# Kernel tuning notes

Measured on AMD Instinct MI355X. Metric: run time of the kernel, lower is better.

Reference implementation:

```python
import jax, jax.numpy as jnp
import numpy as np

B, D, ND, N2, H = 16384, 512, 4, 32, 4
C = D  # attention channels (per-detector feature dim)
EPS = 1e-5


def setup_inputs() -> dict:
    key = jax.random.key(0)
    ks = jax.random.split(key, 8)
    rn = lambda k, s, sc: jax.random.normal(k, s, jnp.float32) * sc
    return {
        'x': jax.random.normal(ks[0], (B, D), jnp.float32),
        'bn1_g': jnp.ones(D * ND, jnp.float32), 'bn1_b': jnp.zeros(D * ND, jnp.float32),
        'w1': rn(ks[1], (ND, D, D), 1e-4),  # diagonal blocks of the masked EnsembleLinear weight
        'bn2_g': jnp.ones(D * ND, jnp.float32), 'bn2_b': jnp.zeros(D * ND, jnp.float32),
        'wq': rn(ks[2], (C, D), 0.02), 'bq': jnp.zeros(C, jnp.float32),
        'wk': rn(ks[3], (C, D), 0.02), 'bk': jnp.zeros(C, jnp.float32),
        'wv': rn(ks[4], (C, D), 0.02), 'bv': jnp.zeros(C, jnp.float32),
        'wo': rn(ks[5], (C, C), 0.02), 'bo': jnp.zeros(C, jnp.float32),
        'ln1_g': jnp.ones(C, jnp.float32), 'ln1_b': jnp.zeros(C, jnp.float32),
        'wff': rn(ks[6], (C, C), 0.02), 'bff': jnp.zeros(C, jnp.float32),
        'ln2_g': jnp.ones(C, jnp.float32), 'ln2_b': jnp.zeros(C, jnp.float32),
        'w2': rn(ks[7], (ND, N2, D), 1e-4),
        'bn3_g': jnp.ones(N2 * ND, jnp.float32), 'bn3_b': jnp.zeros(N2 * ND, jnp.float32),
    }


def _batchnorm(x, g, b):
    # training-mode BatchNorm1d: biased batch stats over the batch axis
    m = x.mean(0)
    v = ((x - m) ** 2).mean(0)
    return (x - m) * jax.lax.rsqrt(v + EPS) * g + b


def _layernorm(x, g, b):
    m = x.mean(-1, keepdims=True)
    v = ((x - m) ** 2).mean(-1, keepdims=True)
    return (x - m) * jax.lax.rsqrt(v + EPS) * g + b


def reference(x, bn1_g, bn1_b, w1, bn2_g, bn2_b, wq, bq, wk, bk, wv, bv, wo, bo,
              ln1_g, ln1_b, wff, bff, ln2_g, ln2_b, w2, bn3_g, bn3_b):
    n = x.shape[0]
    # concat x num_detectors times along features: [n, ND*D]
    xc = jnp.tile(x, (1, ND))
    h = _batchnorm(xc, bn1_g, bn1_b)
    # EnsembleLinear 1: block-diagonal masked matmul == one small GEMM per detector
    h = jnp.einsum('ndi,doi->ndo', h.reshape(n, ND, D), w1).reshape(n, ND * D)
    h = jax.nn.sigmoid(_batchnorm(h, bn2_g, bn2_b))
    # 4-token self-attention over detectors: t is [n, ND, D]
    t = h.reshape(n, ND, D)
    hd = C // H
    q = (t @ wq.T + bq).reshape(n, ND, H, hd).transpose(0, 2, 1, 3)  # [n,H,S,hd]
    k = (t @ wk.T + bk).reshape(n, ND, H, hd).transpose(0, 2, 1, 3)
    v = (t @ wv.T + bv).reshape(n, ND, H, hd).transpose(0, 2, 1, 3)
    scale = jnp.sqrt(jnp.float32(C / H))
    scores = jnp.einsum('nhqd,nhkd->nhqk', q, k) / scale
    attn = jax.nn.softmax(scores, axis=-1)
    o = jnp.einsum('nhqk,nhkd->nhqd', attn, v).transpose(0, 2, 1, 3).reshape(n, ND, C)
    o = o @ wo.T + bo
    a1 = _layernorm(o + t, ln1_g, ln1_b)
    a2 = _layernorm(a1 @ wff.T + bff + a1, ln2_g, ln2_b)
    # EnsembleLinear 2: per-detector D -> N2
    h2 = jnp.einsum('ndi,doi->ndo', a2, w2).reshape(n, ND * N2)
    out = jax.nn.sigmoid(_batchnorm(h2, bn3_g, bn3_b))
    return out
```

## Files before the change

### kernel.cpp

```cpp
#include <hip/hip_runtime.h>
#include <hip/hip_bf16.h>

#define EPS 1e-5f

typedef __attribute__((ext_vector_type(8))) short bf16x8;
typedef __attribute__((ext_vector_type(4))) float f32x4;
typedef __attribute__((ext_vector_type(4))) float float4v;

__device__ __forceinline__ float b2f(short u) {
    union { unsigned int i; float f; } x;
    x.i = ((unsigned int)(unsigned short)u) << 16;
    return x.f;
}
__device__ __forceinline__ short f2b(float f) {
    unsigned int x = __builtin_bit_cast(unsigned int, f);
    unsigned int r = (x + 0x7FFFu + ((x >> 16) & 1u)) >> 16;
    return (short)r;
}

__device__ __forceinline__ void load_lds16(const void* g, void* l) {
    __builtin_amdgcn_global_load_lds(
        (const __attribute__((address_space(1))) unsigned int*)g,
        (__attribute__((address_space(3))) unsigned int*)l, 16, 0, 0);
}


__global__ __launch_bounds__(256) void k_cast_bf16(const float* __restrict__ src,
                                                   short* __restrict__ dst, int n8) {
    int i = blockIdx.x * 256 + threadIdx.x;
    if (i >= n8) return;
    const float4v* s = (const float4v*)src;
    float4v a = s[(long)i * 2], b = s[(long)i * 2 + 1];
    bf16x8 o;
    o[0] = f2b(a[0]); o[1] = f2b(a[1]); o[2] = f2b(a[2]); o[3] = f2b(a[3]);
    o[4] = f2b(b[0]); o[5] = f2b(b[1]); o[6] = f2b(b[2]); o[7] = f2b(b[3]);
    *(bf16x8*)(dst + (long)i * 8) = o;
}

__global__ void k_concat3(const float* __restrict__ a, const float* __restrict__ b,
                          const float* __restrict__ c, float* __restrict__ dst) {
    int i = blockIdx.x * 256 + threadIdx.x;
    if (i < 512) dst[i] = a[i];
    else if (i < 1024) dst[i] = b[i - 512];
    else if (i < 1536) dst[i] = c[i - 1024];
}

__global__ __launch_bounds__(256) void k_stats_x(const float* __restrict__ x,
                                                 float* __restrict__ psum, float* __restrict__ psq) {
    int b = blockIdx.x, tid = threadIdx.x;
    const float* xp = x + (long)b * 64 * 512;
    float s0 = 0, q0 = 0, s1 = 0, q1 = 0;
    for (int r = 0; r < 64; ++r) {
        float v0 = xp[r * 512 + tid];
        float v1 = xp[r * 512 + tid + 256];
        s0 += v0; q0 += v0 * v0; s1 += v1; q1 += v1 * v1;
    }
    psum[b * 512 + tid] = s0; psum[b * 512 + tid + 256] = s1;
    psq[b * 512 + tid] = q0;  psq[b * 512 + tid + 256] = q1;
}


__global__ __launch_bounds__(256) void k_finalize_meanrs(const float* __restrict__ psum,
                                                         const float* __restrict__ psq,
                                                         int nparts, int ncols, float invB,
                                                         float* __restrict__ mean, float* __restrict__ rs) {
    int l = threadIdx.x & 63, grp = threadIdx.x >> 6;
    int c = blockIdx.x * 64 + l;
    float s = 0, q = 0;
    for (int p = grp; p < nparts; p += 4) {
        s += psum[(long)p * ncols + c];
        q += psq[(long)p * ncols + c];
    }
    __shared__ float rs_[4][64], rq_[4][64];
    rs_[grp][l] = s; rq_[grp][l] = q;
    __syncthreads();
    if (grp == 0) {
        s = rs_[0][l] + rs_[1][l] + rs_[2][l] + rs_[3][l];
        q = rq_[0][l] + rq_[1][l] + rq_[2][l] + rq_[3][l];
        float m = s * invB;
        float v = q * invB - m * m;
        mean[c] = m;
        rs[c] = rsqrtf(v + EPS);
    }
}

__global__ __launch_bounds__(256) void k_finalize_ss(const float* __restrict__ psum,
                                                     const float* __restrict__ psq,
                                                     int nparts, int ncols, float invB,
                                                     const float* __restrict__ g, const float* __restrict__ bb,
                                                     float* __restrict__ scale, float* __restrict__ shift) {
    int l = threadIdx.x & 63, grp = threadIdx.x >> 6;
    int c = blockIdx.x * 64 + l;
    float s = 0, q = 0;
    for (int p = grp; p < nparts; p += 4) {
        s += psum[(long)p * ncols + c];
        q += psq[(long)p * ncols + c];
    }
    __shared__ float rs_[4][64], rq_[4][64];
    rs_[grp][l] = s; rq_[grp][l] = q;
    __syncthreads();
    if (grp == 0) {
        s = rs_[0][l] + rs_[1][l] + rs_[2][l] + rs_[3][l];
        q = rq_[0][l] + rq_[1][l] + rq_[2][l] + rq_[3][l];
        float m = s * invB, v = q * invB - m * m;
        float sc = g[c] * rsqrtf(v + EPS);
        scale[c] = sc;
        shift[c] = bb[c] - m * sc;
    }
}

__global__ __launch_bounds__(256) void k_fold_w1(const float* __restrict__ w1, const float* __restrict__ g1,
                                                 const float* __restrict__ b1, const float* __restrict__ mean,
                                                 const float* __restrict__ rs,
                                                 short* __restrict__ W1b, float* __restrict__ beff) {
    int bx = blockIdx.x;
    int d = bx >> 9, tid = threadIdx.x;
    const float* wrow = w1 + (long)bx * 512;
    float part = 0.f;
    for (int i = tid; i < 512; i += 256) {
        float wv = wrow[i];
        float sc = rs[i] * g1[d * 512 + i];
        W1b[(long)bx * 512 + i] = f2b(wv * sc);
        part += (b1[d * 512 + i] - mean[i] * sc) * wv;
    }
    __shared__ float red[256];
    red[tid] = part;
    __syncthreads();
    for (int st = 128; st > 0; st >>= 1) {
        if (tid < st) red[tid] += red[tid + st];
        __syncthreads();
    }
    if (tid == 0) beff[bx] = red[0];
}

__global__ __launch_bounds__(256) void k_stats_h(const short* __restrict__ h,
                                                 float* __restrict__ psum, float* __restrict__ psq) {
    int b = blockIdx.x, tid = threadIdx.x;
    const short* hp = h + (long)b * 64 * 2048;
    float s[8] = {0, 0, 0, 0, 0, 0, 0, 0}, q[8] = {0, 0, 0, 0, 0, 0, 0, 0};
    int c0 = tid * 8;
    for (int r = 0; r < 64; ++r) {
        bf16x8 v = *(const bf16x8*)(hp + r * 2048 + c0);
#pragma unroll
        for (int j = 0; j < 8; ++j) { float f = b2f(v[j]); s[j] += f; q[j] += f * f; }
    }
#pragma unroll
    for (int j = 0; j < 8; ++j) {
        psum[(long)b * 2048 + c0 + j] = s[j];
        psq[(long)b * 2048 + c0 + j] = q[j];
    }
}

__global__ __launch_bounds__(256) void k_bnsig(const short* h, short* t,
                                               const float* __restrict__ scale,
                                               const float* __restrict__ shift) {
    long i8 = ((long)blockIdx.x * 256 + threadIdx.x) * 8;
    int c0 = (int)(i8 & 2047);
    bf16x8 v = *(const bf16x8*)(h + i8);
    bf16x8 o;
#pragma unroll
    for (int j = 0; j < 8; ++j) {
        float x = b2f(v[j]) * scale[c0 + j] + shift[c0 + j];
        o[j] = f2b(1.f / (1.f + __expf(-x)));
    }
    *(bf16x8*)(t + i8) = o;
}

__global__ __launch_bounds__(256) void k_ln(const short* in, short* out,
                                            const float* __restrict__ g, const float* __restrict__ bb) {
    int w = threadIdx.x >> 6, lane = threadIdx.x & 63;
    long row = (long)blockIdx.x * 4 + w;
    const short* rp = in + row * 512;
    bf16x8 v = *(const bf16x8*)(rp + lane * 8);
    float f[8];
    float s = 0.f;
#pragma unroll
    for (int j = 0; j < 8; ++j) { f[j] = b2f(v[j]); s += f[j]; }
#pragma unroll
    for (int m = 1; m < 64; m <<= 1) s += __shfl_xor(s, m, 64);
    float mean = s * (1.f / 512.f);
    float q = 0.f;
#pragma unroll
    for (int j = 0; j < 8; ++j) { float d = f[j] - mean; q += d * d; }
#pragma unroll
    for (int m = 1; m < 64; m <<= 1) q += __shfl_xor(q, m, 64);
    float rs = rsqrtf(q * (1.f / 512.f) + EPS);
    bf16x8 o;
#pragma unroll
    for (int j = 0; j < 8; ++j) {
        int c = lane * 8 + j;
        o[j] = f2b((f[j] - mean) * rs * g[c] + bb[c]);
    }
    *(bf16x8*)(out + row * 512 + lane * 8) = o;
}

__global__ __launch_bounds__(256) void k_stats_o(const float* __restrict__ pre,
                                                 float* __restrict__ psum, float* __restrict__ psq) {
    int b = blockIdx.x, tid = threadIdx.x;
    int c = tid & 127, rh = tid >> 7;
    const float* pp = pre + (long)b * 128 * 128;
    float s = 0, q = 0;
    for (int r = rh; r < 128; r += 2) {
        float v = pp[r * 128 + c];
        s += v; q += v * v;
    }
    psum[(b * 2 + rh) * 128 + c] = s;
    psq[(b * 2 + rh) * 128 + c] = q;
}

__global__ __launch_bounds__(256) void k_bn3sig(const float* __restrict__ pre, float* __restrict__ out,
                                                const float* __restrict__ scale, const float* __restrict__ shift) {
    long i4 = ((long)blockIdx.x * 256 + threadIdx.x) * 4;
    float4v v = *(const float4v*)(pre + i4);
    int c0 = (int)(i4 & 127);
    float4v o;
#pragma unroll
    for (int j = 0; j < 4; ++j) {
        float x = v[j] * scale[c0 + j] + shift[c0 + j];
        o[j] = 1.f / (1.f + __expf(-x));
    }
    *(float4v*)(out + i4) = o;
}


template <int BM, int BN, int WGM, int WGN, bool ADD_RES, bool OUT_BF16>
__global__ __launch_bounds__(WGM* WGN * 64) void k_gemm_bt(
    const short* __restrict__ A, int a_zoff, int lda,
    const short* __restrict__ W, int w_zoff,
    const float* __restrict__ bias, int bias_zoff,
    short* __restrict__ Cb, float* __restrict__ Cf, int c_zoff, int ldc,
    const short* __restrict__ R, int ldr, int K) {
    constexpr int BK = 32;
    constexpr int WM = BM / WGM, WN = BN / WGN;
    constexpr int AM = WM / 16, AN = WN / 16;
    constexpr int NT = WGM * WGN * 64;
    constexpr int CH = (BM + BN) * (BK / 8);

    __shared__ alignas(16) short Smem[(BM + BN) * BK];

    int tid = threadIdx.x;
    int wave = tid >> 6, lane = tid & 63;
    int wm = (wave % WGM) * WM, wn = (wave / WGM) * WN;
    long m0 = (long)blockIdx.x * BM;
    int n0 = blockIdx.y * BN;
    int z = blockIdx.z;
    const short* Az = A + (long)z * a_zoff;
    const short* Wz = W + (long)z * w_zoff;

    f32x4 acc[AM][AN];
#pragma unroll
    for (int i = 0; i < AM; ++i)
#pragma unroll
        for (int j = 0; j < AN; ++j)
#pragma unroll
            for (int q = 0; q < 4; ++q) acc[i][j][q] = 0.f;

    int fr = lane & 15, ko = (lane >> 4) * 8;

    for (int k0 = 0; k0 < K; k0 += BK) {
#pragma unroll
        for (int c = tid; c < CH; c += NT) {
            int row = c >> 2, koff = (c & 3) * 8;
            const short* g = (row < BM) ? (Az + (m0 + row) * lda + k0 + koff)
                                        : (Wz + (long)(n0 + row - BM) * K + k0 + koff);
            load_lds16(g, (char*)Smem + (size_t)c * 16);
        }
        __syncthreads();
        bf16x8 af[AM], bfr[AN];
#pragma unroll
        for (int i = 0; i < AM; ++i) af[i] = *(const bf16x8*)(&Smem[(wm + i * 16 + fr) * BK + ko]);
#pragma unroll
        for (int j = 0; j < AN; ++j) bfr[j] = *(const bf16x8*)(&Smem[(BM + wn + j * 16 + fr) * BK + ko]);
#pragma unroll
        for (int i = 0; i < AM; ++i)
#pragma unroll
            for (int j = 0; j < AN; ++j)
                acc[i][j] = __builtin_amdgcn_mfma_f32_16x16x32_bf16(af[i], bfr[j], acc[i][j], 0, 0, 0);
        __syncthreads();
    }

    int cr = (lane >> 4) * 4, cc = lane & 15;
#pragma unroll
    for (int i = 0; i < AM; ++i) {
#pragma unroll
        for (int j = 0; j < AN; ++j) {
            int col = n0 + wn + j * 16 + cc;
            float bv = bias ? bias[(long)z * bias_zoff + col] : 0.f;
#pragma unroll
            for (int q = 0; q < 4; ++q) {
                long row = m0 + wm + i * 16 + cr + q;
                float v = acc[i][j][q] + bv;
                if constexpr (ADD_RES) v += b2f(R[row * (long)ldr + col]);
                long idx = row * (long)ldc + (long)z * c_zoff + col;
                if constexpr (OUT_BF16) Cb[idx] = f2b(v);
                else Cf[idx] = v;
            }
        }
    }
}

__global__ __launch_bounds__(256) void k_attn(const short* __restrict__ qkv, short* __restrict__ ao) {
    __shared__ alignas(16) short lds[4][4][1544];
    __shared__ float attn_s[4][4][4][4];
    int w = threadIdx.x >> 6, lane = threadIdx.x & 63;
    long n = (long)blockIdx.x * 4 + w;
    const short* src = qkv + n * 4 * 1536;
#pragma unroll
    for (int c = 0; c < 12; ++c) {
        int e = c * 512 + lane * 8;
        *(bf16x8*)(&lds[w][e / 1536][e % 1536]) = *(const bf16x8*)(src + e);
    }
    __syncthreads();
    int h = lane >> 4, a = (lane >> 2) & 3, b = lane & 3;
    const short* qp = &lds[w][a][h * 128];
    const short* kp = &lds[w][b][512 + h * 128];
    float s = 0.f;
#pragma unroll
    for (int j = 0; j < 128; j += 8) {
        bf16x8 qv = *(const bf16x8*)(qp + j);
        bf16x8 kv = *(const bf16x8*)(kp + j);
#pragma unroll
        for (int x = 0; x < 8; ++x) s += b2f(qv[x]) * b2f(kv[x]);
    }
    s *= 0.08838834764831845f;
    float mx = fmaxf(s, __shfl_xor(s, 1, 64));
    mx = fmaxf(mx, __shfl_xor(mx, 2, 64));
    float e = __expf(s - mx);
    float den = e + __shfl_xor(e, 1, 64);
    den += __shfl_xor(den, 2, 64);
    attn_s[w][h][a][b] = e / den;
    __syncthreads();
    int ta = lane >> 4, cg = lane & 15;
#pragma unroll
    for (int hh = 0; hh < 4; ++hh) {
        int c0 = hh * 128 + cg * 8;
        float at0 = attn_s[w][hh][ta][0], at1 = attn_s[w][hh][ta][1];
        float at2 = attn_s[w][hh][ta][2], at3 = attn_s[w][hh][ta][3];
        bf16x8 v0 = *(const bf16x8*)(&lds[w][0][1024 + c0]);
        bf16x8 v1 = *(const bf16x8*)(&lds[w][1][1024 + c0]);
        bf16x8 v2 = *(const bf16x8*)(&lds[w][2][1024 + c0]);
        bf16x8 v3 = *(const bf16x8*)(&lds[w][3][1024 + c0]);
        bf16x8 ov;
#pragma unroll
        for (int j = 0; j < 8; ++j) {
            float val = at0 * b2f(v0[j]) + at1 * b2f(v1[j]) + at2 * b2f(v2[j]) + at3 * b2f(v3[j]);
            ov[j] = f2b(val);
        }
        *(bf16x8*)(ao + (n * 4 + ta) * 512 + c0) = ov;
    }
}


extern "C" void kernel_launch(void* const* d_in, const int* in_sizes, int n_in,
                              void* d_out, int out_size, void* d_ws, size_t ws_size,
                              hipStream_t stream) {
    const float* x = (const float*)d_in[0];
    const float* bn1_g = (const float*)d_in[1];
    const float* bn1_b = (const float*)d_in[2];
    const float* w1 = (const float*)d_in[3];
    const float* bn2_g = (const float*)d_in[4];
    const float* bn2_b = (const float*)d_in[5];
    const float* wq = (const float*)d_in[6];
    const float* bq = (const float*)d_in[7];
    const float* wk = (const float*)d_in[8];
    const float* bk = (const float*)d_in[9];
    const float* wv = (const float*)d_in[10];
    const float* bv = (const float*)d_in[11];
    const float* wo = (const float*)d_in[12];
    const float* bo = (const float*)d_in[13];
    const float* ln1_g = (const float*)d_in[14];
    const float* ln1_b = (const float*)d_in[15];
    const float* wff = (const float*)d_in[16];
    const float* bff = (const float*)d_in[17];
    const float* ln2_g = (const float*)d_in[18];
    const float* ln2_b = (const float*)d_in[19];
    const float* w2 = (const float*)d_in[20];
    const float* bn3_g = (const float*)d_in[21];
    const float* bn3_b = (const float*)d_in[22];
    float* out = (float*)d_out;

    char* ws = (char*)d_ws;
    size_t off = 0;
    auto alloc = [&](size_t bytes) {
        void* p = ws + off;
        off = (off + bytes + 255) & ~(size_t)255;
        return p;
    };

    short* W1b = (short*)alloc(4l * 512 * 512 * 2);
    float* beff = (float*)alloc(4l * 512 * 4);
    short* Wqkvb = (short*)alloc(1536l * 512 * 2);
    float* bqkv = (float*)alloc(1536l * 4);
    short* wo_b = (short*)alloc(512l * 512 * 2);
    short* wff_b = (short*)alloc(512l * 512 * 2);
    short* w2_b = (short*)alloc(4l * 32 * 512 * 2);
    float* mean1 = (float*)alloc(512 * 4);
    float* rs1 = (float*)alloc(512 * 4);
    float* scale2 = (float*)alloc(2048 * 4);
    float* shift2 = (float*)alloc(2048 * 4);
    float* scale3 = (float*)alloc(128 * 4);
    float* shift3 = (float*)alloc(128 * 4);
    float* psum1 = (float*)alloc(256l * 512 * 4);
    float* psq1 = (float*)alloc(256l * 512 * 4);
    float* psum2 = (float*)alloc(256l * 2048 * 4);
    float* psq2 = (float*)alloc(256l * 2048 * 4);
    float* psum3 = (float*)alloc(256l * 128 * 4);
    float* psq3 = (float*)alloc(256l * 128 * 4);
    short* slotA = (short*)alloc(16384l * 2048 * 2);
    float* out_pre = (float*)alloc(16384l * 128 * 4);

    long NC = 1024;
    for (long cand = 16384; cand >= 1024; cand >>= 1) {
        if (off + (size_t)cand * 24576 + (1u << 20) <= ws_size) { NC = cand; break; }
    }
    char* arena = (char*)alloc((size_t)NC * 24576);
    short* xb = (short*)arena;
    short* qkv_c = (short*)arena;
    short* attn_c = (short*)(arena + (size_t)NC * 12288);
    short* a1_c = attn_c + (size_t)NC * 2048;
    short* a2_c = a1_c + (size_t)NC * 2048;

    dim3 B256(256);

    hipLaunchKernelGGL(k_cast_bf16, dim3(4096), B256, 0, stream, x, xb, 8388608 / 8);
    hipLaunchKernelGGL(k_cast_bf16, dim3(128), B256, 0, stream, wq, Wqkvb, 262144 / 8);
    hipLaunchKernelGGL(k_cast_bf16, dim3(128), B256, 0, stream, wk, Wqkvb + 262144, 262144 / 8);
    hipLaunchKernelGGL(k_cast_bf16, dim3(128), B256, 0, stream, wv, Wqkvb + 524288, 262144 / 8);
    hipLaunchKernelGGL(k_cast_bf16, dim3(128), B256, 0, stream, wo, wo_b, 262144 / 8);
    hipLaunchKernelGGL(k_cast_bf16, dim3(128), B256, 0, stream, wff, wff_b, 262144 / 8);
    hipLaunchKernelGGL(k_cast_bf16, dim3(32), B256, 0, stream, w2, w2_b, 65536 / 8);
    hipLaunchKernelGGL(k_concat3, dim3(6), B256, 0, stream, bq, bk, bv, bqkv);

    hipLaunchKernelGGL(k_stats_x, dim3(256), B256, 0, stream, x, psum1, psq1);
    hipLaunchKernelGGL(k_finalize_meanrs, dim3(8), B256, 0, stream, psum1, psq1, 256, 512,
                       1.f / 16384.f, mean1, rs1);
    hipLaunchKernelGGL(k_fold_w1, dim3(2048), B256, 0, stream, w1, bn1_g, bn1_b, mean1, rs1, W1b, beff);

    hipLaunchKernelGGL((k_gemm_bt<128, 128, 2, 2, false, true>), dim3(128, 4, 4), B256, 0, stream,
                       xb, 0, 512, W1b, 512 * 512, beff, 512,
                       slotA, (float*)nullptr, 512, 2048, (const short*)nullptr, 0, 512);

    hipLaunchKernelGGL(k_stats_h, dim3(256), B256, 0, stream, slotA, psum2, psq2);
    hipLaunchKernelGGL(k_finalize_ss, dim3(32), B256, 0, stream, psum2, psq2, 256, 2048,
                       1.f / 16384.f, bn2_g, bn2_b, scale2, shift2);
    hipLaunchKernelGGL(k_bnsig, dim3(16384), B256, 0, stream, slotA, slotA, scale2, shift2);

    long nch = 16384 / NC;
    for (long c = 0; c < nch; ++c) {
        long r0 = c * NC;
        const short* t_c = slotA + r0 * 2048;
        int gx = (int)(NC * 4 / 128);

        hipLaunchKernelGGL((k_gemm_bt<128, 128, 2, 2, false, true>), dim3(gx, 12, 1), B256, 0, stream,
                           t_c, 0, 512, Wqkvb, 0, bqkv, 0,
                           qkv_c, (float*)nullptr, 0, 1536, (const short*)nullptr, 0, 512);

        hipLaunchKernelGGL(k_attn, dim3((int)(NC / 4)), B256, 0, stream, qkv_c, attn_c);

        hipLaunchKernelGGL((k_gemm_bt<128, 128, 2, 2, true, true>), dim3(gx, 4, 1), B256, 0, stream,
                           attn_c, 0, 512, wo_b, 0, bo, 0,
                           a1_c, (float*)nullptr, 0, 512, t_c, 512, 512);

        hipLaunchKernelGGL(k_ln, dim3((int)NC), B256, 0, stream, a1_c, a1_c, ln1_g, ln1_b);

        hipLaunchKernelGGL((k_gemm_bt<128, 128, 2, 2, true, true>), dim3(gx, 4, 1), B256, 0, stream,
                           a1_c, 0, 512, wff_b, 0, bff, 0,
                           a2_c, (float*)nullptr, 0, 512, a1_c, 512, 512);

        hipLaunchKernelGGL(k_ln, dim3((int)NC), B256, 0, stream, a2_c, a2_c, ln2_g, ln2_b);

        hipLaunchKernelGGL((k_gemm_bt<128, 32, 4, 1, false, false>), dim3((int)(NC / 128), 1, 4), B256, 0, stream,
                           a2_c, 512, 2048, w2_b, 32 * 512, (const float*)nullptr, 0,
                           (short*)nullptr, out_pre + r0 * 128, 32, 128, (const short*)nullptr, 0, 512);
    }

    hipLaunchKernelGGL(k_stats_o, dim3(128), B256, 0, stream, out_pre, psum3, psq3);
    hipLaunchKernelGGL(k_finalize_ss, dim3(2), B256, 0, stream, psum3, psq3, 256, 128,
                       1.f / 16384.f, bn3_g, bn3_b, scale3, shift3);
    hipLaunchKernelGGL(k_bn3sig, dim3(2048), B256, 0, stream, out_pre, out, scale3, shift3);
}
```

Before: 657.6 us.

## Fuse BN stats into GEMM epilogues and LayerNorm into full-row GEMMs

Folds the bf16 cast of x into its column-statistics kernel, and computes BN2 partial sums and squares inside a dedicated first-layer GEMM epilogue, which removes the separate pass over h. Adds a full-row (128x512) GEMM kernel with 512 threads that adds bias and residual and applies LayerNorm in its epilogue. This replaces the wo and wff GEMMs plus their standalone LN kernels and removes intermediate round trips through memory. In exchange, the LN kernel keeps a large accumulator set per thread, which may lower occupancy, and it computes the variance as E[x^2]-mean^2 in one pass.

```diff
diff --git a/kernel.cpp b/kernel.cpp
--- a/kernel.cpp
+++ b/kernel.cpp
@@ -45,14 +45,18 @@
     else if (i < 1536) dst[i] = c[i - 1024];
 }
 
-__global__ __launch_bounds__(256) void k_stats_x(const float* __restrict__ x,
-                                                 float* __restrict__ psum, float* __restrict__ psq) {
+__global__ __launch_bounds__(256) void k_statcast_x(const float* __restrict__ x,
+                                                    short* __restrict__ xb,
+                                                    float* __restrict__ psum, float* __restrict__ psq) {
     int b = blockIdx.x, tid = threadIdx.x;
     const float* xp = x + (long)b * 64 * 512;
+    short* xo = xb + (long)b * 64 * 512;
     float s0 = 0, q0 = 0, s1 = 0, q1 = 0;
     for (int r = 0; r < 64; ++r) {
         float v0 = xp[r * 512 + tid];
         float v1 = xp[r * 512 + tid + 256];
+        xo[r * 512 + tid] = f2b(v0);
+        xo[r * 512 + tid + 256] = f2b(v1);
         s0 += v0; q0 += v0 * v0; s1 += v1; q1 += v1 * v1;
     }
     psum[b * 512 + tid] = s0; psum[b * 512 + tid + 256] = s1;
@@ -133,24 +137,6 @@
     if (tid == 0) beff[bx] = red[0];
 }
 
-__global__ __launch_bounds__(256) void k_stats_h(const short* __restrict__ h,
-                                                 float* __restrict__ psum, float* __restrict__ psq) {
-    int b = blockIdx.x, tid = threadIdx.x;
-    const short* hp = h + (long)b * 64 * 2048;
-    float s[8] = {0, 0, 0, 0, 0, 0, 0, 0}, q[8] = {0, 0, 0, 0, 0, 0, 0, 0};
-    int c0 = tid * 8;
-    for (int r = 0; r < 64; ++r) {
-        bf16x8 v = *(const bf16x8*)(hp + r * 2048 + c0);
-#pragma unroll
-        for (int j = 0; j < 8; ++j) { float f = b2f(v[j]); s[j] += f; q[j] += f * f; }
-    }
-#pragma unroll
-    for (int j = 0; j < 8; ++j) {
-        psum[(long)b * 2048 + c0 + j] = s[j];
-        psq[(long)b * 2048 + c0 + j] = q[j];
-    }
-}
-
 __global__ __launch_bounds__(256) void k_bnsig(const short* h, short* t,
                                                const float* __restrict__ scale,
                                                const float* __restrict__ shift) {
@@ -164,34 +150,6 @@
         o[j] = f2b(1.f / (1.f + __expf(-x)));
     }
     *(bf16x8*)(t + i8) = o;
-}
-
-__global__ __launch_bounds__(256) void k_ln(const short* in, short* out,
-                                            const float* __restrict__ g, const float* __restrict__ bb) {
-    int w = threadIdx.x >> 6, lane = threadIdx.x & 63;
-    long row = (long)blockIdx.x * 4 + w;
-    const short* rp = in + row * 512;
-    bf16x8 v = *(const bf16x8*)(rp + lane * 8);
-    float f[8];
-    float s = 0.f;
-#pragma unroll
-    for (int j = 0; j < 8; ++j) { f[j] = b2f(v[j]); s += f[j]; }
-#pragma unroll
-    for (int m = 1; m < 64; m <<= 1) s += __shfl_xor(s, m, 64);
-    float mean = s * (1.f / 512.f);
-    float q = 0.f;
-#pragma unroll
-    for (int j = 0; j < 8; ++j) { float d = f[j] - mean; q += d * d; }
-#pragma unroll
-    for (int m = 1; m < 64; m <<= 1) q += __shfl_xor(q, m, 64);
-    float rs = rsqrtf(q * (1.f / 512.f) + EPS);
-    bf16x8 o;
-#pragma unroll
-    for (int j = 0; j < 8; ++j) {
-        int c = lane * 8 + j;
-        o[j] = f2b((f[j] - mean) * rs * g[c] + bb[c]);
-    }
-    *(bf16x8*)(out + row * 512 + lane * 8) = o;
 }
 
 __global__ __launch_bounds__(256) void k_stats_o(const float* __restrict__ pre,
@@ -223,13 +181,12 @@
 }
 
 
-template <int BM, int BN, int WGM, int WGN, bool ADD_RES, bool OUT_BF16>
+template <int BM, int BN, int WGM, int WGN, bool OUT_BF16>
 __global__ __launch_bounds__(WGM* WGN * 64) void k_gemm_bt(
     const short* __restrict__ A, int a_zoff, int lda,
     const short* __restrict__ W, int w_zoff,
     const float* __restrict__ bias, int bias_zoff,
-    short* __restrict__ Cb, float* __restrict__ Cf, int c_zoff, int ldc,
-    const short* __restrict__ R, int ldr, int K) {
+    short* __restrict__ Cb, float* __restrict__ Cf, int c_zoff, int ldc, int K) {
     constexpr int BK = 32;
     constexpr int WM = BM / WGM, WN = BN / WGN;
     constexpr int AM = WM / 16, AN = WN / 16;
@@ -290,10 +247,183 @@
             for (int q = 0; q < 4; ++q) {
                 long row = m0 + wm + i * 16 + cr + q;
                 float v = acc[i][j][q] + bv;
-                if constexpr (ADD_RES) v += b2f(R[row * (long)ldr + col]);
                 long idx = row * (long)ldc + (long)z * c_zoff + col;
                 if constexpr (OUT_BF16) Cb[idx] = f2b(v);
                 else Cf[idx] = v;
+            }
+        }
+    }
+}
+
+
+__global__ __launch_bounds__(256) void k_gemm_e1(
+    const short* __restrict__ A, const short* __restrict__ W1, const float* __restrict__ beff,
+    short* __restrict__ h, float* __restrict__ psum, float* __restrict__ psq) {
+    constexpr int BK = 32;
+    __shared__ alignas(16) short Smem[256 * BK];
+    __shared__ float cS[2][128], cQ[2][128];
+
+    int tid = threadIdx.x;
+    int wave = tid >> 6, lane = tid & 63;
+    int wm = (wave & 1) * 64, wn = (wave >> 1) * 64;
+    long m0 = (long)blockIdx.x * 128;
+    int n0 = blockIdx.y * 128;
+    int z = blockIdx.z;
+    const short* Wz = W1 + (long)z * 512 * 512;
+
+    f32x4 acc[4][4];
+#pragma unroll
+    for (int i = 0; i < 4; ++i)
+#pragma unroll
+        for (int j = 0; j < 4; ++j)
+#pragma unroll
+            for (int q = 0; q < 4; ++q) acc[i][j][q] = 0.f;
+
+    int fr = lane & 15, ko = (lane >> 4) * 8;
+
+    for (int k0 = 0; k0 < 512; k0 += BK) {
+#pragma unroll
+        for (int c = tid; c < 1024; c += 256) {
+            int row = c >> 2, koff = (c & 3) * 8;
+            const short* g = (row < 128) ? (A + (m0 + row) * 512 + k0 + koff)
+                                         : (Wz + (long)(n0 + row - 128) * 512 + k0 + koff);
+            load_lds16(g, (char*)Smem + (size_t)c * 16);
+        }
+        __syncthreads();
+        bf16x8 af[4], bfr[4];
+#pragma unroll
+        for (int i = 0; i < 4; ++i) af[i] = *(const bf16x8*)(&Smem[(wm + i * 16 + fr) * BK + ko]);
+#pragma unroll
+        for (int j = 0; j < 4; ++j) bfr[j] = *(const bf16x8*)(&Smem[(128 + wn + j * 16 + fr) * BK + ko]);
+#pragma unroll
+        for (int i = 0; i < 4; ++i)
+#pragma unroll
+            for (int j = 0; j < 4; ++j)
+                acc[i][j] = __builtin_amdgcn_mfma_f32_16x16x32_bf16(af[i], bfr[j], acc[i][j], 0, 0, 0);
+        __syncthreads();
+    }
+
+    int cr = (lane >> 4) * 4, cc = lane & 15;
+#pragma unroll
+    for (int j = 0; j < 4; ++j) {
+        int cl = wn + j * 16 + cc;
+        float bv = beff[z * 512 + n0 + cl];
+        float s = 0.f, qq = 0.f;
+#pragma unroll
+        for (int i = 0; i < 4; ++i)
+#pragma unroll
+            for (int q = 0; q < 4; ++q) {
+                float v = acc[i][j][q] + bv;
+                acc[i][j][q] = v;
+                s += v; qq += v * v;
+                long row = m0 + wm + i * 16 + cr + q;
+                h[row * 2048 + z * 512 + n0 + cl] = f2b(v);
+            }
+        s += __shfl_xor(s, 16, 64); s += __shfl_xor(s, 32, 64);
+        qq += __shfl_xor(qq, 16, 64); qq += __shfl_xor(qq, 32, 64);
+        if (lane < 16) { cS[wave & 1][cl] = s; cQ[wave & 1][cl] = qq; }
+    }
+    __syncthreads();
+    if (tid < 128) {
+        float S = cS[0][tid] + cS[1][tid];
+        float Q = cQ[0][tid] + cQ[1][tid];
+        psum[(long)blockIdx.x * 2048 + z * 512 + n0 + tid] = S;
+        psq[(long)blockIdx.x * 2048 + z * 512 + n0 + tid] = Q;
+    }
+}
+
+
+__global__ __launch_bounds__(512) void k_gemm_ln(
+    const short* __restrict__ A, const short* __restrict__ W,
+    const float* __restrict__ bias, const short* __restrict__ R,
+    const float* __restrict__ g, const float* __restrict__ bb,
+    short* __restrict__ out) {
+    constexpr int BK = 32;
+    __shared__ alignas(16) short Smem[(128 + 512) * BK];
+    __shared__ float lnS[128][4], lnQ[128][4];
+
+    int tid = threadIdx.x;
+    int wave = tid >> 6, lane = tid & 63;
+    int wm = (wave & 1) * 64;
+    int wc = wave >> 1;
+    int wn = wc * 128;
+    long m0 = (long)blockIdx.x * 128;
+
+    f32x4 acc[4][8];
+#pragma unroll
+    for (int i = 0; i < 4; ++i)
+#pragma unroll
+        for (int j = 0; j < 8; ++j)
+#pragma unroll
+            for (int q = 0; q < 4; ++q) acc[i][j][q] = 0.f;
+
+    int fr = lane & 15, ko = (lane >> 4) * 8;
+
+    for (int k0 = 0; k0 < 512; k0 += BK) {
+#pragma unroll
+        for (int c = tid; c < 2560; c += 512) {
+            int row = c >> 2, koff = (c & 3) * 8;
+            const short* gp = (row < 128) ? (A + (m0 + row) * 512 + k0 + koff)
+                                          : (W + (long)(row - 128) * 512 + k0 + koff);
+            load_lds16(gp, (char*)Smem + (size_t)c * 16);
+        }
+        __syncthreads();
+        bf16x8 af[4], bfr[8];
+#pragma unroll
+        for (int i = 0; i < 4; ++i) af[i] = *(const bf16x8*)(&Smem[(wm + i * 16 + fr) * BK + ko]);
+#pragma unroll
+        for (int j = 0; j < 8; ++j) bfr[j] = *(const bf16x8*)(&Smem[(128 + wn + j * 16 + fr) * BK + ko]);
+#pragma unroll
+        for (int i = 0; i < 4; ++i)
+#pragma unroll
+            for (int j = 0; j < 8; ++j)
+                acc[i][j] = __builtin_amdgcn_mfma_f32_16x16x32_bf16(af[i], bfr[j], acc[i][j], 0, 0, 0);
+        __syncthreads();
+    }
+
+    int cr = (lane >> 4) * 4, cc = lane & 15;
+    float bj[8];
+#pragma unroll
+    for (int j = 0; j < 8; ++j) bj[j] = bias[wn + j * 16 + cc];
+
+#pragma unroll
+    for (int i = 0; i < 4; ++i) {
+#pragma unroll
+        for (int q = 0; q < 4; ++q) {
+            long row = m0 + wm + i * 16 + cr + q;
+            float s = 0.f, qq = 0.f;
+#pragma unroll
+            for (int j = 0; j < 8; ++j) {
+                float v = acc[i][j][q] + bj[j] + b2f(R[row * 512 + wn + j * 16 + cc]);
+                acc[i][j][q] = v;
+                s += v; qq += v * v;
+            }
+            s += __shfl_xor(s, 1, 64); qq += __shfl_xor(qq, 1, 64);
+            s += __shfl_xor(s, 2, 64); qq += __shfl_xor(qq, 2, 64);
+            s += __shfl_xor(s, 4, 64); qq += __shfl_xor(qq, 4, 64);
+            s += __shfl_xor(s, 8, 64); qq += __shfl_xor(qq, 8, 64);
+            if (cc == 0) {
+                int rl = wm + i * 16 + cr + q;
+                lnS[rl][wc] = s;
+                lnQ[rl][wc] = qq;
+            }
+        }
+    }
+    __syncthreads();
+#pragma unroll
+    for (int i = 0; i < 4; ++i) {
+#pragma unroll
+        for (int q = 0; q < 4; ++q) {
+            int rl = wm + i * 16 + cr + q;
+            float S = lnS[rl][0] + lnS[rl][1] + lnS[rl][2] + lnS[rl][3];
+            float Q = lnQ[rl][0] + lnQ[rl][1] + lnQ[rl][2] + lnQ[rl][3];
+            float mean = S * (1.f / 512.f);
+            float rstd = rsqrtf(Q * (1.f / 512.f) - mean * mean + EPS);
+            long row = m0 + rl;
+#pragma unroll
+            for (int j = 0; j < 8; ++j) {
+                int col = wn + j * 16 + cc;
+                out[row * 512 + col] = f2b((acc[i][j][q] - mean) * rstd * g[col] + bb[col]);
             }
         }
     }
@@ -402,8 +532,8 @@
     float* shift3 = (float*)alloc(128 * 4);
     float* psum1 = (float*)alloc(256l * 512 * 4);
     float* psq1 = (float*)alloc(256l * 512 * 4);
-    float* psum2 = (float*)alloc(256l * 2048 * 4);
-    float* psq2 = (float*)alloc(256l * 2048 * 4);
+    float* psum2 = (float*)alloc(128l * 2048 * 4);
+    float* psq2 = (float*)alloc(128l * 2048 * 4);
     float* psum3 = (float*)alloc(256l * 128 * 4);
     float* psq3 = (float*)alloc(256l * 128 * 4);
     short* slotA = (short*)alloc(16384l * 2048 * 2);
@@ -422,7 +552,7 @@
 
     dim3 B256(256);
 
-    hipLaunchKernelGGL(k_cast_bf16, dim3(4096), B256, 0, stream, x, xb, 8388608 / 8);
+    hipLaunchKernelGGL(k_statcast_x, dim3(256), B256, 0, stream, x, xb, psum1, psq1);
     hipLaunchKernelGGL(k_cast_bf16, dim3(128), B256, 0, stream, wq, Wqkvb, 262144 / 8);
     hipLaunchKernelGGL(k_cast_bf16, dim3(128), B256, 0, stream, wk, Wqkvb + 262144, 262144 / 8);
     hipLaunchKernelGGL(k_cast_bf16, dim3(128), B256, 0, stream, wv, Wqkvb + 524288, 262144 / 8);
@@ -431,17 +561,14 @@
     hipLaunchKernelGGL(k_cast_bf16, dim3(32), B256, 0, stream, w2, w2_b, 65536 / 8);
     hipLaunchKernelGGL(k_concat3, dim3(6), B256, 0, stream, bq, bk, bv, bqkv);
 
-    hipLaunchKernelGGL(k_stats_x, dim3(256), B256, 0, stream, x, psum1, psq1);
     hipLaunchKernelGGL(k_finalize_meanrs, dim3(8), B256, 0, stream, psum1, psq1, 256, 512,
                        1.f / 16384.f, mean1, rs1);
     hipLaunchKernelGGL(k_fold_w1, dim3(2048), B256, 0, stream, w1, bn1_g, bn1_b, mean1, rs1, W1b, beff);
 
-    hipLaunchKernelGGL((k_gemm_bt<128, 128, 2, 2, false, true>), dim3(128, 4, 4), B256, 0, stream,
-                       xb, 0, 512, W1b, 512 * 512, beff, 512,
-                       slotA, (float*)nullptr, 512, 2048, (const short*)nullptr, 0, 512);
-
-    hipLaunchKernelGGL(k_stats_h, dim3(256), B256, 0, stream, slotA, psum2, psq2);
-    hipLaunchKernelGGL(k_finalize_ss, dim3(32), B256, 0, stream, psum2, psq2, 256, 2048,
+    hipLaunchKernelGGL(k_gemm_e1, dim3(128, 4, 4), B256, 0, stream,
+                       xb, W1b, beff, slotA, psum2, psq2);
+
+    hipLaunchKernelGGL(k_finalize_ss, dim3(32), B256, 0, stream, psum2, psq2, 128, 2048,
                        1.f / 16384.f, bn2_g, bn2_b, scale2, shift2);
     hipLaunchKernelGGL(k_bnsig, dim3(16384), B256, 0, stream, slotA, slotA, scale2, shift2);
 
@@ -451,27 +578,21 @@
         const short* t_c = slotA + r0 * 2048;
         int gx = (int)(NC * 4 / 128);
 
-        hipLaunchKernelGGL((k_gemm_bt<128, 128, 2, 2, false, true>), dim3(gx, 12, 1), B256, 0, stream,
+        hipLaunchKernelGGL((k_gemm_bt<128, 128, 2, 2, true>), dim3(gx, 12, 1), B256, 0, stream,
                            t_c, 0, 512, Wqkvb, 0, bqkv, 0,
-                           qkv_c, (float*)nullptr, 0, 1536, (const short*)nullptr, 0, 512);
+                           qkv_c, (float*)nullptr, 0, 1536, 512);
 
         hipLaunchKernelGGL(k_attn, dim3((int)(NC / 4)), B256, 0, stream, qkv_c, attn_c);
 
-        hipLaunchKernelGGL((k_gemm_bt<128, 128, 2, 2, true, true>), dim3(gx, 4, 1), B256, 0, stream,
-                           attn_c, 0, 512, wo_b, 0, bo, 0,
-                           a1_c, (float*)nullptr, 0, 512, t_c, 512, 512);
-
-        hipLaunchKernelGGL(k_ln, dim3((int)NC), B256, 0, stream, a1_c, a1_c, ln1_g, ln1_b);
-
-        hipLaunchKernelGGL((k_gemm_bt<128, 128, 2, 2, true, true>), dim3(gx, 4, 1), B256, 0, stream,
-                           a1_c, 0, 512, wff_b, 0, bff, 0,
-                           a2_c, (float*)nullptr, 0, 512, a1_c, 512, 512);
-
-        hipLaunchKernelGGL(k_ln, dim3((int)NC), B256, 0, stream, a2_c, a2_c, ln2_g, ln2_b);
-
-        hipLaunchKernelGGL((k_gemm_bt<128, 32, 4, 1, false, false>), dim3((int)(NC / 128), 1, 4), B256, 0, stream,
+        hipLaunchKernelGGL(k_gemm_ln, dim3(gx), dim3(512), 0, stream,
+                           attn_c, wo_b, bo, t_c, ln1_g, ln1_b, a1_c);
+
+        hipLaunchKernelGGL(k_gemm_ln, dim3(gx), dim3(512), 0, stream,
+                           a1_c, wff_b, bff, a1_c, ln2_g, ln2_b, a2_c);
+
+        hipLaunchKernelGGL((k_gemm_bt<128, 32, 4, 1, false>), dim3((int)(NC / 128), 1, 4), B256, 0, stream,
                            a2_c, 512, 2048, w2_b, 32 * 512, (const float*)nullptr, 0,
-                           (short*)nullptr, out_pre + r0 * 128, 32, 128, (const short*)nullptr, 0, 512);
+                           (short*)nullptr, out_pre + r0 * 128, 32, 128, 512);
     }
 
     hipLaunchKernelGGL(k_stats_o, dim3(128), B256, 0, stream, out_pre, psum3, psq3);
```

Result: slower. 722.5 us (+9.9%).

## Fuse BN batch statistics into x cast and first ensemble GEMM epilogue

Applied to the files above, without the earlier changes.

Merges the x bf16 cast with the BN1 column-statistics pass so x is read once. Replaces the generic first GEMM plus separate h-statistics kernel with a dedicated GEMM whose epilogue computes per-block column sums and sums of squares, removing a full re-read of the 16384x2048 activation. It also caps the attention chunk size at 8192 rows. Statistics now come from fp32 values before bf16 rounding, and the custom GEMM may schedule differently from the templated one.

```diff
diff --git a/kernel.cpp b/kernel.cpp
--- a/kernel.cpp
+++ b/kernel.cpp
@@ -45,14 +45,18 @@
     else if (i < 1536) dst[i] = c[i - 1024];
 }
 
-__global__ __launch_bounds__(256) void k_stats_x(const float* __restrict__ x,
-                                                 float* __restrict__ psum, float* __restrict__ psq) {
+__global__ __launch_bounds__(256) void k_statcast_x(const float* __restrict__ x,
+                                                    short* __restrict__ xb,
+                                                    float* __restrict__ psum, float* __restrict__ psq) {
     int b = blockIdx.x, tid = threadIdx.x;
     const float* xp = x + (long)b * 64 * 512;
+    short* xo = xb + (long)b * 64 * 512;
     float s0 = 0, q0 = 0, s1 = 0, q1 = 0;
     for (int r = 0; r < 64; ++r) {
         float v0 = xp[r * 512 + tid];
         float v1 = xp[r * 512 + tid + 256];
+        xo[r * 512 + tid] = f2b(v0);
+        xo[r * 512 + tid + 256] = f2b(v1);
         s0 += v0; q0 += v0 * v0; s1 += v1; q1 += v1 * v1;
     }
     psum[b * 512 + tid] = s0; psum[b * 512 + tid + 256] = s1;
@@ -133,24 +137,6 @@
     if (tid == 0) beff[bx] = red[0];
 }
 
-__global__ __launch_bounds__(256) void k_stats_h(const short* __restrict__ h,
-                                                 float* __restrict__ psum, float* __restrict__ psq) {
-    int b = blockIdx.x, tid = threadIdx.x;
-    const short* hp = h + (long)b * 64 * 2048;
-    float s[8] = {0, 0, 0, 0, 0, 0, 0, 0}, q[8] = {0, 0, 0, 0, 0, 0, 0, 0};
-    int c0 = tid * 8;
-    for (int r = 0; r < 64; ++r) {
-        bf16x8 v = *(const bf16x8*)(hp + r * 2048 + c0);
-#pragma unroll
-        for (int j = 0; j < 8; ++j) { float f = b2f(v[j]); s[j] += f; q[j] += f * f; }
-    }
-#pragma unroll
-    for (int j = 0; j < 8; ++j) {
-        psum[(long)b * 2048 + c0 + j] = s[j];
-        psq[(long)b * 2048 + c0 + j] = q[j];
-    }
-}
-
 __global__ __launch_bounds__(256) void k_bnsig(const short* h, short* t,
                                                const float* __restrict__ scale,
                                                const float* __restrict__ shift) {
@@ -296,6 +282,96 @@
                 else Cf[idx] = v;
             }
         }
+    }
+}
+
+
+__global__ __launch_bounds__(256) void k_gemm_e1(
+    const short* __restrict__ A, const short* __restrict__ W1, const float* __restrict__ beff,
+    short* __restrict__ h, float* __restrict__ psum, float* __restrict__ psq) {
+    constexpr int BK = 32;
+    __shared__ alignas(16) short Smem[256 * BK];
+    __shared__ float cS[2][128], cQ[2][128];
+
+    int tid = threadIdx.x;
+    int wave = tid >> 6, lane = tid & 63;
+    int wm = (wave & 1) * 64, wn = (wave >> 1) * 64;
+    long m0 = (long)blockIdx.x * 128;
+    int n0 = blockIdx.y * 128;
+    int z = blockIdx.z;
+    const short* Wz = W1 + (long)z * 512 * 512;
+
+    f32x4 acc[4][4];
+#pragma unroll
+    for (int i = 0; i < 4; ++i)
+#pragma unroll
+        for (int j = 0; j < 4; ++j)
+#pragma unroll
+            for (int q = 0; q < 4; ++q) acc[i][j][q] = 0.f;
+
+    int fr = lane & 15, ko = (lane >> 4) * 8;
+
+    for (int k0 = 0; k0 < 512; k0 += BK) {
+#pragma unroll
+        for (int c = tid; c < 1024; c += 256) {
+            int row = c >> 2, koff = (c & 3) * 8;
+            const short* g = (row < 128) ? (A + (m0 + row) * 512 + k0 + koff)
+                                         : (Wz + (long)(n0 + row - 128) * 512 + k0 + koff);
+            load_lds16(g, (char*)Smem + (size_t)c * 16);
+        }
+        __syncthreads();
+        bf16x8 af[4], bfr[4];
+#pragma unroll
+        for (int i = 0; i < 4; ++i) af[i] = *(const bf16x8*)(&Smem[(wm + i * 16 + fr) * BK + ko]);
+#pragma unroll
+        for (int j = 0; j < 4; ++j) bfr[j] = *(const bf16x8*)(&Smem[(128 + wn + j * 16 + fr) * BK + ko]);
+#pragma unroll
+        for (int i = 0; i < 4; ++i)
+#pragma unroll
+            for (int j = 0; j < 4; ++j)
+                acc[i][j] = __builtin_amdgcn_mfma_f32_16x16x32_bf16(af[i], bfr[j], acc[i][j], 0, 0, 0);
+        __syncthreads();
+    }
+
+    int cr = (lane >> 4) * 4, cc = lane & 15;
+    float bv[4], colS[4], colQ[4];
+#pragma unroll
+    for (int j = 0; j < 4; ++j) {
+        bv[j] = beff[z * 512 + n0 + wn + j * 16 + cc];
+        colS[j] = 0.f; colQ[j] = 0.f;
+    }
+#pragma unroll
+    for (int i = 0; i < 4; ++i)
+#pragma unroll
+        for (int j = 0; j < 4; ++j)
+#pragma unroll
+            for (int q = 0; q < 4; ++q) {
+                float v = acc[i][j][q] + bv[j];
+                acc[i][j][q] = v;
+                colS[j] += v; colQ[j] += v * v;
+            }
+#pragma unroll
+    for (int i = 0; i < 4; ++i)
+#pragma unroll
+        for (int q = 0; q < 4; ++q) {
+            long row = m0 + wm + i * 16 + cr + q;
+            short* hp = h + row * 2048 + z * 512 + n0 + wn + cc;
+#pragma unroll
+            for (int j = 0; j < 4; ++j) hp[j * 16] = f2b(acc[i][j][q]);
+        }
+#pragma unroll
+    for (int j = 0; j < 4; ++j) {
+        float s = colS[j], qq = colQ[j];
+        s += __shfl_xor(s, 16, 64); s += __shfl_xor(s, 32, 64);
+        qq += __shfl_xor(qq, 16, 64); qq += __shfl_xor(qq, 32, 64);
+        if (lane < 16) { cS[wave & 1][wn + j * 16 + cc] = s; cQ[wave & 1][wn + j * 16 + cc] = qq; }
+    }
+    __syncthreads();
+    if (tid < 128) {
+        float S = cS[0][tid] + cS[1][tid];
+        float Q = cQ[0][tid] + cQ[1][tid];
+        psum[(long)blockIdx.x * 2048 + z * 512 + n0 + tid] = S;
+        psq[(long)blockIdx.x * 2048 + z * 512 + n0 + tid] = Q;
     }
 }
 
@@ -402,15 +478,15 @@
     float* shift3 = (float*)alloc(128 * 4);
     float* psum1 = (float*)alloc(256l * 512 * 4);
     float* psq1 = (float*)alloc(256l * 512 * 4);
-    float* psum2 = (float*)alloc(256l * 2048 * 4);
-    float* psq2 = (float*)alloc(256l * 2048 * 4);
+    float* psum2 = (float*)alloc(128l * 2048 * 4);
+    float* psq2 = (float*)alloc(128l * 2048 * 4);
     float* psum3 = (float*)alloc(256l * 128 * 4);
     float* psq3 = (float*)alloc(256l * 128 * 4);
     short* slotA = (short*)alloc(16384l * 2048 * 2);
     float* out_pre = (float*)alloc(16384l * 128 * 4);
 
     long NC = 1024;
-    for (long cand = 16384; cand >= 1024; cand >>= 1) {
+    for (long cand = 8192; cand >= 1024; cand >>= 1) {
         if (off + (size_t)cand * 24576 + (1u << 20) <= ws_size) { NC = cand; break; }
     }
     char* arena = (char*)alloc((size_t)NC * 24576);
@@ -422,7 +498,7 @@
 
     dim3 B256(256);
 
-    hipLaunchKernelGGL(k_cast_bf16, dim3(4096), B256, 0, stream, x, xb, 8388608 / 8);
+    hipLaunchKernelGGL(k_statcast_x, dim3(256), B256, 0, stream, x, xb, psum1, psq1);
     hipLaunchKernelGGL(k_cast_bf16, dim3(128), B256, 0, stream, wq, Wqkvb, 262144 / 8);
     hipLaunchKernelGGL(k_cast_bf16, dim3(128), B256, 0, stream, wk, Wqkvb + 262144, 262144 / 8);
     hipLaunchKernelGGL(k_cast_bf16, dim3(128), B256, 0, stream, wv, Wqkvb + 524288, 262144 / 8);
@@ -431,17 +507,14 @@
     hipLaunchKernelGGL(k_cast_bf16, dim3(32), B256, 0, stream, w2, w2_b, 65536 / 8);
     hipLaunchKernelGGL(k_concat3, dim3(6), B256, 0, stream, bq, bk, bv, bqkv);
 
-    hipLaunchKernelGGL(k_stats_x, dim3(256), B256, 0, stream, x, psum1, psq1);
     hipLaunchKernelGGL(k_finalize_meanrs, dim3(8), B256, 0, stream, psum1, psq1, 256, 512,
                        1.f / 16384.f, mean1, rs1);
     hipLaunchKernelGGL(k_fold_w1, dim3(2048), B256, 0, stream, w1, bn1_g, bn1_b, mean1, rs1, W1b, beff);
 
-    hipLaunchKernelGGL((k_gemm_bt<128, 128, 2, 2, false, true>), dim3(128, 4, 4), B256, 0, stream,
-                       xb, 0, 512, W1b, 512 * 512, beff, 512,
-                       slotA, (float*)nullptr, 512, 2048, (const short*)nullptr, 0, 512);
-
-    hipLaunchKernelGGL(k_stats_h, dim3(256), B256, 0, stream, slotA, psum2, psq2);
-    hipLaunchKernelGGL(k_finalize_ss, dim3(32), B256, 0, stream, psum2, psq2, 256, 2048,
+    hipLaunchKernelGGL(k_gemm_e1, dim3(128, 4, 4), B256, 0, stream,
+                       xb, W1b, beff, slotA, psum2, psq2);
+
+    hipLaunchKernelGGL(k_finalize_ss, dim3(32), B256, 0, stream, psum2, psq2, 128, 2048,
                        1.f / 16384.f, bn2_g, bn2_b, scale2, shift2);
     hipLaunchKernelGGL(k_bnsig, dim3(16384), B256, 0, stream, slotA, slotA, scale2, shift2);
 
```

New measurement: 629.0 us. 4.4% less time.
